# Kernel optimization log

Measured on AMD Instinct MI355X. Metric: run time of the kernel, lower is better.

Reference implementation:

```python
import jax, jax.numpy as jnp
import numpy as np

# MUCMA: multiuser CMA adaptive MIMO FIR equalizer (commplax af.mucma)
# framed_signal: (N, taps, dims) complex, carried as re/im float32 pairs.
N, TAPS, DIMS, DELTA = 131072, 19, 2, 6
LR = 2.0 ** (-13)
BETA = 0.999
R2 = 1.32  # E|a|^4 / E|a|^2 for unit-power 16QAM constellation


def setup_inputs() -> dict:
    key = jax.random.key(0)
    k1, k2 = jax.random.split(key)
    fr_re = jax.random.normal(k1, (N, TAPS, DIMS), dtype=jnp.float32) * 0.7071
    fr_im = jax.random.normal(k2, (N, TAPS, DIMS), dtype=jnp.float32) * 0.7071
    # initial MIMO weights: identity at the center tap (commplax mucma init)
    w0_re = np.zeros((DIMS, DIMS, TAPS), dtype=np.float32)
    ctap = (TAPS + 1) // 2 - 1
    w0_re[np.arange(DIMS), np.arange(DIMS), ctap] = 1.0
    return {
        'fr_re': fr_re,
        'fr_im': fr_im,
        'w0_re': jnp.asarray(w0_re),
        'w0_im': jnp.zeros((DIMS, DIMS, TAPS), jnp.float32),
    }


def _mucma_forward(fr_re, fr_im, w0_re, w0_im):
    u_all = fr_re + 1j * fr_im                      # (N, taps, dims) complex64
    w0 = (w0_re + 1j * w0_im).astype(u_all.dtype)   # (dims, dims, taps)
    # mask kills self cross-correlation terms (k == l)
    mask = (1.0 - jnp.eye(DIMS, dtype=jnp.float32))[:, :, None]

    def step(carry, u):
        # u: (taps, dims) frame of input samples
        w, z, r, bp = carry
        v = jnp.einsum('ijt,tj->i', w, u)                     # MIMO FIR output, (dims,)
        z = jnp.concatenate((v[None, :], z[:-1]))             # output delay line, (delta, dims)
        # running cross-correlation r[k,l,d] ~ E[z_k(n) z_l(n-d)^*]
        r = BETA * r + (1.0 - BETA) * jnp.einsum('k,dl->kld', v, z.conj())
        rhat = (r / (1.0 - bp)) * mask                        # bias-corrected, off-diagonal only
        e = R2 - jnp.abs(v) ** 2                              # CMA modulus error, (dims,) real
        loss = jnp.sum(e ** 2) + 2.0 * jnp.sum(jnp.abs(rhat) ** 2)
        uc = u.conj().T[None, :, :]                           # (1, dims, taps)
        g_cma = -2.0 * e[:, None, None] * v[:, None, None] * uc
        g_mu = 2.0 * jnp.einsum('kld,dl->k', rhat, z.conj())[:, None, None] * uc
        w_new = w - LR * (g_cma + g_mu)
        bp = bp * BETA
        # emit the weights USED for this symbol (pre-update), as commplax does
        return (w_new, z, r, bp), (w, loss)

    z0 = jnp.zeros((DELTA, DIMS), u_all.dtype)
    r0 = jnp.zeros((DIMS, DIMS, DELTA), u_all.dtype)
    carry0 = (w0, z0, r0, jnp.float32(BETA))
    _, (ws, _losses) = jax.lax.scan(step, carry0, u_all)
    # apply: per-symbol MIMO filtering with the recorded weight trace
    sig = jnp.einsum('nijt,ntj->ni', ws, u_all)               # (N, dims) complex
    return jnp.stack([sig.real, sig.imag], axis=-1)           # (N, dims, 2) float32


def reference(fr_re, fr_im, w0_re, w0_im):
    return _mucma_forward(fr_re, fr_im, w0_re, w0_im)
```

## Files before the change

### kernel.cpp

```cpp
#include <hip/hip_runtime.h>


typedef float v2f __attribute__((ext_vector_type(2)));
typedef float v4f __attribute__((ext_vector_type(4), aligned(4)));

constexpr int   NTAPS  = 19;
constexpr int   FRST   = 38;
constexpr float BETA_C = 0.999f;
constexpr float OMB_C  = 0.001f;
constexpr float LR_C   = 0.0001220703125f;
constexpr float R2_C   = 1.32f;

template <int CTRL>
__device__ __forceinline__ float dpp_add(float x) {
    return x + __int_as_float(__builtin_amdgcn_update_dpp(
        0, __float_as_int(x), CTRL, 0xF, 0xF, true));
}
template <int CTRL>
__device__ __forceinline__ float dpp_mov(float x) {
    return __int_as_float(__builtin_amdgcn_update_dpp(
        0, __float_as_int(x), CTRL, 0xF, 0xF, true));
}
__device__ __forceinline__ float rowred_bcast(float x) {
    x = dpp_add<0x121>(x);
    x = dpp_add<0x122>(x);
    x = dpp_add<0x124>(x);
    x = dpp_add<0x128>(x);
    return x;
}
__device__ __forceinline__ void plane32_swap(float& a, float& b) {
    asm("s_nop 1\n\t"
        "v_permlane32_swap_b32 %0, %1\n\t"
        "s_nop 1"
        : "+v"(a), "+v"(b));
}

__global__ void __launch_bounds__(64, 1)
mucma_scan_kernel(const float* __restrict__ fr_re, const float* __restrict__ fr_im,
                  const float* __restrict__ w0r_in, const float* __restrict__ w0i_in,
                  float* __restrict__ out, int nsym)
{
    const int  lane = threadIdx.x;
    const int  sl   = lane & 31;
    const int  h    = lane >> 5;
    const int  loff = (4 * sl < 34) ? 4 * sl : 34;
    const float mA  = (sl <= 8) ? 1.f : 0.f;
    const float mB  = (sl <= 9) ? 1.f : 0.f;
    const bool d0f  = (sl == 10);
    const bool stf  = (sl == 0);

    v2f wA_r = {0.f,0.f}, wA_i = {0.f,0.f}, wB_r = {0.f,0.f}, wB_i = {0.f,0.f};
    if (sl <= 8) {
        const int b = h * FRST + 2 * sl;
        wA_r.x = w0r_in[b];         wA_r.y = w0r_in[b + NTAPS];
        wA_i.x = w0i_in[b];         wA_i.y = w0i_in[b + NTAPS];
        wB_r.x = w0r_in[b + 1];     wB_r.y = w0r_in[b + NTAPS + 1];
        wB_i.x = w0i_in[b + 1];     wB_i.y = w0i_in[b + NTAPS + 1];
    } else if (sl == 9) {
        wB_r.x = w0r_in[h * FRST + 18];  wB_r.y = w0r_in[h * FRST + 37];
        wB_i.x = w0i_in[h * FRST + 18];  wB_i.y = w0i_in[h * FRST + 37];
    }
    float r_re = 0.f, r_im = 0.f, z_re = 0.f, z_im = 0.f;
    float bp = BETA_C;

    bool csel;
    {
        const float own = h ? 11.f : 7.f;
        float v = own, X = own;
        plane32_swap(X, v);
        csel = (X != own);
    }

    const float* pre = fr_re + loff;
    const float* pim = fr_im + loff;

    v4f rr[8], ri[8];
#pragma unroll
    for (int p = 0; p < 8; ++p) {
        const int idx = (p < nsym) ? p : (nsym - 1);
        rr[p] = *(const v4f*)(pre + (size_t)idx * FRST);
        ri[p] = *(const v4f*)(pim + (size_t)idx * FRST);
    }

    auto body = [&](int n, int p, int npf) {
        const v4f uR = rr[p], uI = ri[p];
        rr[p] = *(const v4f*)(pre + (size_t)npf * FRST);
        ri[p] = *(const v4f*)(pim + (size_t)npf * FRST);

        const v2f uA_r = {uR.x, uR.y}, uB_r = {uR.z, uR.w};
        const v2f uA_i = {uI.x, uI.y}, uB_i = {uI.z, uI.w};

        v2f tr = wA_r * uA_r - wA_i * uA_i + wB_r * uB_r - wB_i * uB_i;
        v2f ti = wA_r * uA_i + wA_i * uA_r + wB_r * uB_i + wB_i * uB_r;
        float xr = tr.x + tr.y;
        float xi = ti.x + ti.y;
        xr = rowred_bcast(xr);
        xi = rowred_bcast(xi);
        const float vkr = xr, vki = xi;

        float Xr = xr, Xi = xi;
        plane32_swap(Xr, xr);
        plane32_swap(Xi, xi);
        const float vlr = csel ? Xr : xr;
        const float vli = csel ? Xi : xi;

        const float zsr = dpp_mov<0x111>(z_re);
        const float zsi = dpp_mov<0x111>(z_im);
        z_re = d0f ? vlr : zsr;
        z_im = d0f ? vli : zsi;

        const float ar = OMB_C * vkr, ai = OMB_C * vki;
        r_re = BETA_C * r_re + (ar * z_re + ai * z_im);
        r_im = BETA_C * r_im + (ai * z_re - ar * z_im);

        float qr = r_re * z_re + r_im * z_im;
        float qi = r_im * z_re - r_re * z_im;
        qr = rowred_bcast(qr);
        qi = rowred_bcast(qi);

        const float inv = __builtin_amdgcn_rcpf(1.0f - bp);
        bp *= BETA_C;
        const float i2 = (2.0f * LR_C) * inv;
        const float ek = R2_C - (vkr * vkr + vki * vki);
        const float e2 = (-2.0f * LR_C) * ek;
        const float cr = e2 * vkr + i2 * qr;
        const float ci = e2 * vki + i2 * qi;

        const float crA = cr * mA, ciA = ci * mA;
        const float crB = cr * mB, ciB = ci * mB;
        const v2f cAr = {crA, crA}, cAi = {ciA, ciA};
        const v2f cBr = {crB, crB}, cBi = {ciB, ciB};
        wA_r -= cAr * uA_r + cAi * uA_i;
        wA_i -= cAi * uA_r - cAr * uA_i;
        wB_r -= cBr * uB_r + cBi * uB_i;
        wB_i -= cBi * uB_r - cBr * uB_i;

        if (stf) {
            v2f o; o.x = vkr; o.y = vki;
            *(v2f*)(out + 4 * (size_t)n + 2 * h) = o;
        }
    };

    int NBmain = nsym / 8 - 1;
    if (NBmain < 0) NBmain = 0;
    for (int b = 0; b < NBmain; ++b) {
        const int nb = b * 8;
#pragma unroll
        for (int p = 0; p < 8; ++p) body(nb + p, p, nb + p + 8);
    }
    for (int nb = NBmain * 8; nb < nsym; nb += 8) {
#pragma unroll
        for (int p = 0; p < 8; ++p) {
            const int n = nb + p;
            if (n < nsym) {
                int npf = n + 8;
                if (npf > nsym - 1) npf = nsym - 1;
                body(n, p, npf);
            }
        }
    }
}

extern "C" void kernel_launch(void* const* d_in, const int* in_sizes, int n_in,
                              void* d_out, int out_size, void* d_ws, size_t ws_size,
                              hipStream_t stream)
{
    const float* fr_re = (const float*)d_in[0];
    const float* fr_im = (const float*)d_in[1];
    const float* w0r   = (const float*)d_in[2];
    const float* w0i   = (const float*)d_in[3];
    float* outp = (float*)d_out;
    const int nsym = in_sizes[0] / FRST;
    hipLaunchKernelGGL(mucma_scan_kernel, dim3(1), dim3(64), 0, stream,
                       fr_re, fr_im, w0r, w0i, outp, nsym);
}
```

Measured before the change: 29.79 ms.

## Precompute frame Gram correlations to pipeline FIR output across scan steps

Adds a parallel pre-pass that computes the inner product between consecutive input frames, S[n] = <u_n, u_{n+1}>. The scan then computes the next symbol's FIR output from the pre-update weights and corrects it algebraically with the rank-one update term (c * S), which takes the reduction for v off the serial dependency chain. After SPLIT_N steps it also drops the bias-correction reciprocal, treating 1/(1-beta^n) as 1. That shortcut is an approximation whose error depends on the step count, and the new pre-pass is an extra kernel launch that needs workspace memory.

New measurement: 29.66 ms. Within noise of the previous version (-0.4%).

```diff
diff --git a/kernel.cpp b/kernel.cpp
--- a/kernel.cpp
+++ b/kernel.cpp
@@ -2,14 +2,15 @@
 
 
 typedef float v2f __attribute__((ext_vector_type(2)));
-typedef float v4f __attribute__((ext_vector_type(4), aligned(4)));
-
-constexpr int   NTAPS  = 19;
-constexpr int   FRST   = 38;
-constexpr float BETA_C = 0.999f;
-constexpr float OMB_C  = 0.001f;
-constexpr float LR_C   = 0.0001220703125f;
-constexpr float R2_C   = 1.32f;
+typedef float v4f __attribute__((ext_vector_type(4), aligned(8)));
+
+constexpr int   NTAPS   = 19;
+constexpr int   FRST    = 38;
+constexpr float BETA_C  = 0.999f;
+constexpr float OMB_C   = 0.001f;
+constexpr float LR_C    = 0.0001220703125f;
+constexpr float R2_C    = 1.32f;
+constexpr int   SPLIT_N = 24576;
 
 template <int CTRL>
 __device__ __forceinline__ float dpp_add(float x) {
@@ -34,130 +35,220 @@
         "s_nop 1"
         : "+v"(a), "+v"(b));
 }
+__device__ __forceinline__ void plane32_swap2(float& a, float& b, float& c, float& d) {
+    asm("s_nop 1\n\t"
+        "v_permlane32_swap_b32 %0, %1\n\t"
+        "v_permlane32_swap_b32 %2, %3\n\t"
+        "s_nop 1"
+        : "+v"(a), "+v"(b), "+v"(c), "+v"(d));
+}
+
+__global__ void __launch_bounds__(64)
+gram_kernel(const float* __restrict__ fr_re, const float* __restrict__ fr_im,
+            v2f* __restrict__ S, int nsym)
+{
+    __shared__ float lre[65 * FRST], lim[65 * FRST];
+    const int lane = threadIdx.x;
+    const int n0   = blockIdx.x * 64;
+    const int gmax = nsym * FRST;
+    for (int idx = lane; idx < 65 * FRST; idx += 64) {
+        const int g = n0 * FRST + idx;
+        if (g < gmax) { lre[idx] = fr_re[g]; lim[idx] = fr_im[g]; }
+    }
+    __syncthreads();
+    const int n = n0 + lane;
+    if (n >= nsym) return;
+    v2f s = {0.f, 0.f};
+    if (n + 1 < nsym) {
+        const float* ar = lre + lane * FRST;
+        const float* ai = lim + lane * FRST;
+        const float* br = ar + FRST;
+        const float* bi = ai + FRST;
+#pragma unroll
+        for (int e = 0; e < FRST; ++e) {
+            s.x += ar[e] * br[e] + ai[e] * bi[e];
+            s.y += ar[e] * bi[e] - ai[e] * br[e];
+        }
+    }
+    S[n] = s;
+}
+
+struct LaneCtx {
+    const float* pre; const float* pim; const v2f* Sb; float* out;
+    float mA, mB; bool d0f, stf, csel; int h;
+};
+struct ScanSt {
+    v2f  wA_r, wA_i, wB_r, wB_i;
+    float r_re, r_im, z_re, z_im, bp;
+    float Ar, Ai;
+    float cpr, cpi;
+    v2f  sp;
+    v4f  rr[8], ri[8];
+    v2f  sr[8];
+};
+
+template <bool EARLY, int P>
+__device__ __forceinline__ void mstep(int n, int npf, const LaneCtx& L, ScanSt& s)
+{
+    constexpr int PN = (P + 1) & 7;
+    const v4f uR  = s.rr[P],  uI  = s.ri[P];
+    const v4f u1R = s.rr[PN], u1I = s.ri[PN];
+    s.rr[P] = *(const v4f*)(L.pre + (size_t)npf * FRST);
+    s.ri[P] = *(const v4f*)(L.pim + (size_t)npf * FRST);
+    const v2f Scur = s.sr[P];
+    s.sr[P] = L.Sb[npf];
+
+    const v2f uA_r = {u1R.x, u1R.y}, uB_r = {u1R.z, u1R.w};
+    const v2f uA_i = {u1I.x, u1I.y}, uB_i = {u1I.z, u1I.w};
+    v2f tr = s.wA_r * uA_r - s.wA_i * uA_i + s.wB_r * uB_r - s.wB_i * uB_i;
+    v2f ti = s.wA_r * uA_i + s.wA_i * uA_r + s.wB_r * uB_i + s.wB_i * uB_r;
+    float nAr = tr.x + tr.y;
+    float nAi = ti.x + ti.y;
+    nAr = rowred_bcast(nAr);
+    nAi = rowred_bcast(nAi);
+
+    const float vkr = s.Ar - (s.cpr * s.sp.x - s.cpi * s.sp.y);
+    const float vki = s.Ai - (s.cpr * s.sp.y + s.cpi * s.sp.x);
+
+    if (L.stf) {
+        v2f o; o.x = vkr; o.y = vki;
+        *(v2f*)(L.out + 4 * (size_t)n + 2 * L.h) = o;
+    }
+
+    float Xr = vkr, Yr = vkr, Xi = vki, Yi = vki;
+    plane32_swap2(Xr, Yr, Xi, Yi);
+    const float vlr = L.csel ? Xr : Yr;
+    const float vli = L.csel ? Xi : Yi;
+
+    const float zsr = dpp_mov<0x111>(s.z_re);
+    const float zsi = dpp_mov<0x111>(s.z_im);
+    s.z_re = L.d0f ? vlr : zsr;
+    s.z_im = L.d0f ? vli : zsi;
+
+    const float ar = OMB_C * vkr, ai = OMB_C * vki;
+    s.r_re = BETA_C * s.r_re + (ar * s.z_re + ai * s.z_im);
+    s.r_im = BETA_C * s.r_im + (ai * s.z_re - ar * s.z_im);
+
+    float qr = s.r_re * s.z_re + s.r_im * s.z_im;
+    float qi = s.r_im * s.z_re - s.r_re * s.z_im;
+    qr = rowred_bcast(qr);
+    qi = rowred_bcast(qi);
+
+    float i2;
+    if (EARLY) {
+        const float inv = __builtin_amdgcn_rcpf(1.0f - s.bp);
+        s.bp *= BETA_C;
+        i2 = (2.0f * LR_C) * inv;
+    } else {
+        i2 = 2.0f * LR_C;
+    }
+    const float t  = vkr * vkr + vki * vki;
+    const float e2 = fmaf(2.0f * LR_C, t, -(2.0f * LR_C) * R2_C);
+    const float cr = fmaf(e2, vkr, i2 * qr);
+    const float ci = fmaf(e2, vki, i2 * qi);
+
+    const float crA = cr * L.mA, ciA = ci * L.mA;
+    const float crB = cr * L.mB, ciB = ci * L.mB;
+    const v2f uA_r0 = {uR.x, uR.y}, uB_r0 = {uR.z, uR.w};
+    const v2f uA_i0 = {uI.x, uI.y}, uB_i0 = {uI.z, uI.w};
+    const v2f cAr = {crA, crA}, cAi = {ciA, ciA};
+    const v2f cBr = {crB, crB}, cBi = {ciB, ciB};
+    s.wA_r -= cAr * uA_r0 + cAi * uA_i0;
+    s.wA_i -= cAi * uA_r0 - cAr * uA_i0;
+    s.wB_r -= cBr * uB_r0 + cBi * uB_i0;
+    s.wB_i -= cBi * uB_r0 - cBr * uB_i0;
+
+    s.Ar = nAr; s.Ai = nAi; s.cpr = cr; s.cpi = ci; s.sp = Scur;
+}
+
+template <bool EARLY>
+__device__ __forceinline__ void block8(int nb, const LaneCtx& L, ScanSt& s) {
+    mstep<EARLY, 0>(nb + 0, nb + 8,  L, s);
+    mstep<EARLY, 1>(nb + 1, nb + 9,  L, s);
+    mstep<EARLY, 2>(nb + 2, nb + 10, L, s);
+    mstep<EARLY, 3>(nb + 3, nb + 11, L, s);
+    mstep<EARLY, 4>(nb + 4, nb + 12, L, s);
+    mstep<EARLY, 5>(nb + 5, nb + 13, L, s);
+    mstep<EARLY, 6>(nb + 6, nb + 14, L, s);
+    mstep<EARLY, 7>(nb + 7, nb + 15, L, s);
+}
+template <bool EARLY>
+__device__ __forceinline__ void block8c(int nb, int nsym, const LaneCtx& L, ScanSt& s) {
+    const int last = nsym - 1;
+#define STEPC(K) { const int n = nb + K; if (n < nsym) { \
+        int npf = n + 8; if (npf > last) npf = last; mstep<EARLY, K>(n, npf, L, s); } }
+    STEPC(0) STEPC(1) STEPC(2) STEPC(3) STEPC(4) STEPC(5) STEPC(6) STEPC(7)
+#undef STEPC
+}
 
 __global__ void __launch_bounds__(64, 1)
 mucma_scan_kernel(const float* __restrict__ fr_re, const float* __restrict__ fr_im,
                   const float* __restrict__ w0r_in, const float* __restrict__ w0i_in,
-                  float* __restrict__ out, int nsym)
-{
-    const int  lane = threadIdx.x;
-    const int  sl   = lane & 31;
-    const int  h    = lane >> 5;
-    const int  loff = (4 * sl < 34) ? 4 * sl : 34;
-    const float mA  = (sl <= 8) ? 1.f : 0.f;
-    const float mB  = (sl <= 9) ? 1.f : 0.f;
-    const bool d0f  = (sl == 10);
-    const bool stf  = (sl == 0);
-
-    v2f wA_r = {0.f,0.f}, wA_i = {0.f,0.f}, wB_r = {0.f,0.f}, wB_i = {0.f,0.f};
-    if (sl <= 8) {
-        const int b = h * FRST + 2 * sl;
-        wA_r.x = w0r_in[b];         wA_r.y = w0r_in[b + NTAPS];
-        wA_i.x = w0i_in[b];         wA_i.y = w0i_in[b + NTAPS];
-        wB_r.x = w0r_in[b + 1];     wB_r.y = w0r_in[b + NTAPS + 1];
-        wB_i.x = w0i_in[b + 1];     wB_i.y = w0i_in[b + NTAPS + 1];
-    } else if (sl == 9) {
-        wB_r.x = w0r_in[h * FRST + 18];  wB_r.y = w0r_in[h * FRST + 37];
-        wB_i.x = w0i_in[h * FRST + 18];  wB_i.y = w0i_in[h * FRST + 37];
-    }
-    float r_re = 0.f, r_im = 0.f, z_re = 0.f, z_im = 0.f;
-    float bp = BETA_C;
-
-    bool csel;
+                  const v2f* __restrict__ Sbuf, float* __restrict__ out, int nsym)
+{
+    const int lane = threadIdx.x;
+    const int sl   = lane & 31;
+    const int h    = lane >> 5;
+    const int loff = (4 * sl < 34) ? 4 * sl : 34;
+
+    LaneCtx L;
+    L.pre = fr_re + loff;  L.pim = fr_im + loff;  L.Sb = Sbuf;  L.out = out;
+    L.mA  = (sl <= 8) ? 1.f : 0.f;
+    L.mB  = (sl <= 9) ? 1.f : 0.f;
+    L.d0f = (sl == 10);
+    L.stf = (sl == 0);
+    L.h   = h;
     {
         const float own = h ? 11.f : 7.f;
         float v = own, X = own;
         plane32_swap(X, v);
-        csel = (X != own);
-    }
-
-    const float* pre = fr_re + loff;
-    const float* pim = fr_im + loff;
-
-    v4f rr[8], ri[8];
+        L.csel = (X != own);
+    }
+
+    ScanSt s;
+    s.wA_r = {0.f,0.f}; s.wA_i = {0.f,0.f}; s.wB_r = {0.f,0.f}; s.wB_i = {0.f,0.f};
+    if (sl <= 8) {
+        const int b = h * FRST + 2 * sl;
+        s.wA_r.x = w0r_in[b];       s.wA_r.y = w0r_in[b + NTAPS];
+        s.wA_i.x = w0i_in[b];       s.wA_i.y = w0i_in[b + NTAPS];
+        s.wB_r.x = w0r_in[b + 1];   s.wB_r.y = w0r_in[b + NTAPS + 1];
+        s.wB_i.x = w0i_in[b + 1];   s.wB_i.y = w0i_in[b + NTAPS + 1];
+    } else if (sl == 9) {
+        s.wB_r.x = w0r_in[h * FRST + 18];  s.wB_r.y = w0r_in[h * FRST + 37];
+        s.wB_i.x = w0i_in[h * FRST + 18];  s.wB_i.y = w0i_in[h * FRST + 37];
+    }
+    s.r_re = 0.f; s.r_im = 0.f; s.z_re = 0.f; s.z_im = 0.f;
+    s.bp = BETA_C;
+    s.cpr = 0.f; s.cpi = 0.f; s.sp = {0.f, 0.f};
+
 #pragma unroll
     for (int p = 0; p < 8; ++p) {
         const int idx = (p < nsym) ? p : (nsym - 1);
-        rr[p] = *(const v4f*)(pre + (size_t)idx * FRST);
-        ri[p] = *(const v4f*)(pim + (size_t)idx * FRST);
-    }
-
-    auto body = [&](int n, int p, int npf) {
-        const v4f uR = rr[p], uI = ri[p];
-        rr[p] = *(const v4f*)(pre + (size_t)npf * FRST);
-        ri[p] = *(const v4f*)(pim + (size_t)npf * FRST);
-
+        s.rr[p] = *(const v4f*)(L.pre + (size_t)idx * FRST);
+        s.ri[p] = *(const v4f*)(L.pim + (size_t)idx * FRST);
+        s.sr[p] = Sbuf[idx];
+    }
+    {
+        const v4f uR = s.rr[0], uI = s.ri[0];
         const v2f uA_r = {uR.x, uR.y}, uB_r = {uR.z, uR.w};
         const v2f uA_i = {uI.x, uI.y}, uB_i = {uI.z, uI.w};
-
-        v2f tr = wA_r * uA_r - wA_i * uA_i + wB_r * uB_r - wB_i * uB_i;
-        v2f ti = wA_r * uA_i + wA_i * uA_r + wB_r * uB_i + wB_i * uB_r;
-        float xr = tr.x + tr.y;
-        float xi = ti.x + ti.y;
-        xr = rowred_bcast(xr);
-        xi = rowred_bcast(xi);
-        const float vkr = xr, vki = xi;
-
-        float Xr = xr, Xi = xi;
-        plane32_swap(Xr, xr);
-        plane32_swap(Xi, xi);
-        const float vlr = csel ? Xr : xr;
-        const float vli = csel ? Xi : xi;
-
-        const float zsr = dpp_mov<0x111>(z_re);
-        const float zsi = dpp_mov<0x111>(z_im);
-        z_re = d0f ? vlr : zsr;
-        z_im = d0f ? vli : zsi;
-
-        const float ar = OMB_C * vkr, ai = OMB_C * vki;
-        r_re = BETA_C * r_re + (ar * z_re + ai * z_im);
-        r_im = BETA_C * r_im + (ai * z_re - ar * z_im);
-
-        float qr = r_re * z_re + r_im * z_im;
-        float qi = r_im * z_re - r_re * z_im;
-        qr = rowred_bcast(qr);
-        qi = rowred_bcast(qi);
-
-        const float inv = __builtin_amdgcn_rcpf(1.0f - bp);
-        bp *= BETA_C;
-        const float i2 = (2.0f * LR_C) * inv;
-        const float ek = R2_C - (vkr * vkr + vki * vki);
-        const float e2 = (-2.0f * LR_C) * ek;
-        const float cr = e2 * vkr + i2 * qr;
-        const float ci = e2 * vki + i2 * qi;
-
-        const float crA = cr * mA, ciA = ci * mA;
-        const float crB = cr * mB, ciB = ci * mB;
-        const v2f cAr = {crA, crA}, cAi = {ciA, ciA};
-        const v2f cBr = {crB, crB}, cBi = {ciB, ciB};
-        wA_r -= cAr * uA_r + cAi * uA_i;
-        wA_i -= cAi * uA_r - cAr * uA_i;
-        wB_r -= cBr * uB_r + cBi * uB_i;
-        wB_i -= cBi * uB_r - cBr * uB_i;
-
-        if (stf) {
-            v2f o; o.x = vkr; o.y = vki;
-            *(v2f*)(out + 4 * (size_t)n + 2 * h) = o;
-        }
-    };
-
-    int NBmain = nsym / 8 - 1;
-    if (NBmain < 0) NBmain = 0;
-    for (int b = 0; b < NBmain; ++b) {
-        const int nb = b * 8;
-#pragma unroll
-        for (int p = 0; p < 8; ++p) body(nb + p, p, nb + p + 8);
-    }
-    for (int nb = NBmain * 8; nb < nsym; nb += 8) {
-#pragma unroll
-        for (int p = 0; p < 8; ++p) {
-            const int n = nb + p;
-            if (n < nsym) {
-                int npf = n + 8;
-                if (npf > nsym - 1) npf = nsym - 1;
-                body(n, p, npf);
-            }
-        }
+        v2f tr = s.wA_r * uA_r - s.wA_i * uA_i + s.wB_r * uB_r - s.wB_i * uB_i;
+        v2f ti = s.wA_r * uA_i + s.wA_i * uA_r + s.wB_r * uB_i + s.wB_i * uB_r;
+        s.Ar = rowred_bcast(tr.x + tr.y);
+        s.Ai = rowred_bcast(ti.x + ti.y);
+    }
+
+    if (nsym >= SPLIT_N + 16) {
+        for (int nb = 0; nb < SPLIT_N; nb += 8)
+            block8<true>(nb, L, s);
+        const int nmain = (nsym - 8) & ~7;
+        for (int nb = SPLIT_N; nb < nmain; nb += 8)
+            block8<false>(nb, L, s);
+        for (int nb = nmain; nb < nsym; nb += 8)
+            block8c<false>(nb, nsym, L, s);
+    } else {
+        for (int nb = 0; nb < nsym; nb += 8)
+            block8c<true>(nb, nsym, L, s);
     }
 }
 
@@ -170,7 +261,11 @@
     const float* w0r   = (const float*)d_in[2];
     const float* w0i   = (const float*)d_in[3];
     float* outp = (float*)d_out;
+    v2f*   Sbuf = (v2f*)d_ws;
     const int nsym = in_sizes[0] / FRST;
+
+    hipLaunchKernelGGL(gram_kernel, dim3((nsym + 63) / 64), dim3(64), 0, stream,
+                       fr_re, fr_im, Sbuf, nsym);
     hipLaunchKernelGGL(mucma_scan_kernel, dim3(1), dim3(64), 0, stream,
-                       fr_re, fr_im, w0r, w0i, outp, nsym);
-}
+                       fr_re, fr_im, w0r, w0i, Sbuf, outp, nsym);
+}
```

## Split sequential scan into two pipelined waves using precomputed frame Gram terms

Applied to the files above, without the earlier changes.

Adds a parallel pre-pass that computes lagged inner products between consecutive input frames (lags 1-3). The serial scan then runs as two wavefronts. One wave applies the filter with weights that lag by a few symbols and corrects the output using those inner products and the recent update coefficients. The other wave does the error, cross-correlation and coefficient work, and the two hand values to each other through LDS rings with a barrier per symbol. This is meant to take the weight update and filter reduction off the critical serial dependency chain. After SPLIT_N symbols it also drops the bias-correction reciprocal, treating 1-bp as 1, which is only approximately exact. It needs workspace, and the per-step barrier adds synchronisation cost.

New measurement: 29.44 ms. About the same (-1.2%).

```diff
diff --git a/kernel.cpp b/kernel.cpp
--- a/kernel.cpp
+++ b/kernel.cpp
@@ -1,15 +1,17 @@
 #include <hip/hip_runtime.h>
+#include <stdint.h>
 
 
 typedef float v2f __attribute__((ext_vector_type(2)));
-typedef float v4f __attribute__((ext_vector_type(4), aligned(4)));
-
-constexpr int   NTAPS  = 19;
-constexpr int   FRST   = 38;
-constexpr float BETA_C = 0.999f;
-constexpr float OMB_C  = 0.001f;
-constexpr float LR_C   = 0.0001220703125f;
-constexpr float R2_C   = 1.32f;
+typedef float v4f __attribute__((ext_vector_type(4), aligned(8)));
+
+constexpr int   NTAPS   = 19;
+constexpr int   FRST    = 38;
+constexpr float BETA_C  = 0.999f;
+constexpr float OMB_C   = 0.001f;
+constexpr float LR_C    = 0.0001220703125f;
+constexpr float R2_C    = 1.32f;
+constexpr int   SPLIT_N = 24576;
 
 template <int CTRL>
 __device__ __forceinline__ float dpp_add(float x) {
@@ -34,11 +36,316 @@
         "s_nop 1"
         : "+v"(a), "+v"(b));
 }
+__device__ __forceinline__ void plane32_swap2(float& a, float& b, float& c, float& d) {
+    asm("s_nop 1\n\t"
+        "v_permlane32_swap_b32 %0, %1\n\t"
+        "v_permlane32_swap_b32 %2, %3\n\t"
+        "s_nop 1"
+        : "+v"(a), "+v"(b), "+v"(c), "+v"(d));
+}
+__device__ __forceinline__ void wg_barrier() {
+    asm volatile("s_waitcnt lgkmcnt(0)\n\ts_barrier" ::: "memory");
+}
+
+__global__ void __launch_bounds__(64)
+gram3_kernel(const float* __restrict__ fr_re, const float* __restrict__ fr_im,
+             char* __restrict__ ws, int nsym)
+{
+    v4f* SA4 = (v4f*)ws;
+    v2f* SA2 = (v2f*)(ws + (size_t)nsym * 16);
+    __shared__ float lre[67 * FRST], lim[67 * FRST];
+    const int lane = threadIdx.x;
+    const int n0   = blockIdx.x * 64;
+    const long gmax = (long)nsym * FRST;
+    for (int idx = lane; idx < 67 * FRST; idx += 64) {
+        const long g = (long)n0 * FRST + idx;
+        if (g < gmax) { lre[idx] = fr_re[g]; lim[idx] = fr_im[g]; }
+    }
+    __syncthreads();
+    const int n = n0 + lane;
+    if (n >= nsym) return;
+    const float* ar = lre + lane * FRST;
+    const float* ai = lim + lane * FRST;
+    v2f s1 = {0.f,0.f}, s2 = {0.f,0.f}, s3 = {0.f,0.f};
+#pragma unroll
+    for (int e = 0; e < FRST; ++e) {
+        const float xr = ar[e], xi = ai[e];
+        const float b1r = ar[e+FRST],   b1i = ai[e+FRST];
+        const float b2r = ar[e+2*FRST], b2i = ai[e+2*FRST];
+        const float b3r = ar[e+3*FRST], b3i = ai[e+3*FRST];
+        s1.x += xr*b1r + xi*b1i;  s1.y += xr*b1i - xi*b1r;
+        s2.x += xr*b2r + xi*b2i;  s2.y += xr*b2i - xi*b2r;
+        s3.x += xr*b3r + xi*b3i;  s3.y += xr*b3i - xi*b3r;
+    }
+    if (n + 1 >= nsym) s1 = (v2f){0.f,0.f};
+    if (n + 2 >= nsym) s2 = (v2f){0.f,0.f};
+    if (n + 3 >= nsym) s3 = (v2f){0.f,0.f};
+    SA4[n] = (v4f){s1.x, s1.y, s2.x, s2.y};
+    SA2[n] = s3;
+}
+
+struct AS {
+    float araw_r, araw_i;
+    float cp1r, cp1i, cp2r, cp2i, cp3r, cp3i;
+    float z_re, z_im, r_re, r_im, bp;
+    v4f sa4[8]; v2f sa2[8];
+    const v4f* pa40; const v2f* pa20;
+    const v4f* pa4;  const v2f* pa2;
+    float* stb; int stadv;
+};
+
+template <bool EARLY, int P>
+__device__ __forceinline__ void A_step(AS& s, const v4f* p4, const v2f* p2,
+                                       float* sp, float* cw, const float* ard,
+                                       bool d0f, bool csel)
+{
+    const v4f S1e = s.sa4[(P+7)&7];
+    const v4f S2e = s.sa4[(P+6)&7];
+    const v2f S3e = s.sa2[(P+5)&7];
+
+    float vr = s.araw_r - (s.cp1r*S1e.x - s.cp1i*S1e.y)
+                        - (s.cp2r*S2e.z - s.cp2i*S2e.w)
+                        - (s.cp3r*S3e.x - s.cp3i*S3e.y);
+    float vi = s.araw_i - (s.cp1r*S1e.y + s.cp1i*S1e.x)
+                        - (s.cp2r*S2e.w + s.cp2i*S2e.z)
+                        - (s.cp3r*S3e.y + s.cp3i*S3e.x);
+
+    const v2f an = *(const v2f*)(ard + ((P+1)&7)*4);
+
+    *(v2f*)sp = (v2f){vr, vi};
+
+    float Xr = vr, Yr = vr, Xi = vi, Yi = vi;
+    plane32_swap2(Xr, Yr, Xi, Yi);
+    const float vlr = csel ? Xr : Yr;
+    const float vli = csel ? Xi : Yi;
+
+    const float zsr = dpp_mov<0x111>(s.z_re);
+    const float zsi = dpp_mov<0x111>(s.z_im);
+    s.z_re = d0f ? vlr : zsr;
+    s.z_im = d0f ? vli : zsi;
+
+    const float ar = OMB_C * vr, ai = OMB_C * vi;
+    s.r_re = BETA_C * s.r_re + (ar * s.z_re + ai * s.z_im);
+    s.r_im = BETA_C * s.r_im + (ai * s.z_re - ar * s.z_im);
+
+    float qr = s.r_re * s.z_re + s.r_im * s.z_im;
+    float qi = s.r_im * s.z_re - s.r_re * s.z_im;
+    qr = rowred_bcast(qr);
+    qi = rowred_bcast(qi);
+
+    float i2;
+    if (EARLY) {
+        const float inv = __builtin_amdgcn_rcpf(1.0f - s.bp);
+        s.bp *= BETA_C;
+        i2 = (2.0f * LR_C) * inv;
+    } else {
+        i2 = 2.0f * LR_C;
+    }
+    const float t  = vr*vr + vi*vi;
+    const float e2 = fmaf(2.0f*LR_C, t, -(2.0f*LR_C)*R2_C);
+    const float cr = fmaf(e2, vr, i2*qr);
+    const float ci = fmaf(e2, vi, i2*qi);
+
+    *(v2f*)(cw + P*4) = (v2f){cr, ci};
+
+    s.cp3r = s.cp2r; s.cp3i = s.cp2i;
+    s.cp2r = s.cp1r; s.cp2i = s.cp1i;
+    s.cp1r = cr;     s.cp1i = ci;
+    s.araw_r = an.x; s.araw_i = an.y;
+
+    s.sa4[(P+5)&7] = p4[0];
+    s.sa2[(P+5)&7] = p2[0];
+}
+
+template <bool EARLY, bool TAIL>
+__device__ __forceinline__ void a_block(AS& s, int nb, int last,
+    float* cw, const float* ard, bool d0f, bool csel, float* gdl)
+{
+#define ASTP(P) { \
+    const v4f* p4; const v2f* p2; float* sp; \
+    if (TAIL) { int rfi = nb + P + 5; if (rfi > last) rfi = last; \
+                p4 = s.pa40 + rfi; p2 = s.pa20 + rfi; \
+                sp = (nb + P <= last) ? (s.stb + P*4) : (gdl + P*4); } \
+    else { p4 = s.pa4 + (P+5); p2 = s.pa2 + (P+5); sp = s.stb + P*4; } \
+    A_step<EARLY, P>(s, p4, p2, sp, cw, ard, d0f, csel); \
+    wg_barrier(); }
+    ASTP(0) ASTP(1) ASTP(2) ASTP(3) ASTP(4) ASTP(5) ASTP(6) ASTP(7)
+#undef ASTP
+    s.pa4 += 8; s.pa2 += 8; s.stb += s.stadv;
+}
+
+struct BS {
+    v2f wA_r, wA_i, wB_r, wB_i;
+    v4f rr[8], ri[8];
+    v4f uo_r, uo_i;
+    float cregr, cregi;
+    const float* ubr; const float* ubi;
+    float mA, mB;
+};
+
+__device__ __forceinline__ v2f b_tree(const BS& s, const v4f& uR, const v4f& uI) {
+    const v2f uA_r = {uR.x,uR.y}, uB_r = {uR.z,uR.w};
+    const v2f uA_i = {uI.x,uI.y}, uB_i = {uI.z,uI.w};
+    v2f tr = s.wA_r*uA_r - s.wA_i*uA_i + s.wB_r*uB_r - s.wB_i*uB_i;
+    v2f ti = s.wA_r*uA_i + s.wA_i*uA_r + s.wB_r*uB_i + s.wB_i*uB_r;
+    return (v2f){ rowred_bcast(tr.x + tr.y), rowred_bcast(ti.x + ti.y) };
+}
+
+template <int P>
+__device__ __forceinline__ void B_step(BS& s, const float* urf_re, const float* urf_im,
+                                       const float* crd, float* aw)
+{
+    const v2f cn = *(const v2f*)(crd + ((P+7)&7)*4);
+
+    const float crA = s.cregr * s.mA, ciA = s.cregi * s.mA;
+    const float crB = s.cregr * s.mB, ciB = s.cregi * s.mB;
+    {
+        const v2f uA_r = {s.uo_r.x, s.uo_r.y}, uB_r = {s.uo_r.z, s.uo_r.w};
+        const v2f uA_i = {s.uo_i.x, s.uo_i.y}, uB_i = {s.uo_i.z, s.uo_i.w};
+        s.wA_r -= (v2f){crA,crA}*uA_r + (v2f){ciA,ciA}*uA_i;
+        s.wA_i -= (v2f){ciA,ciA}*uA_r - (v2f){crA,crA}*uA_i;
+        s.wB_r -= (v2f){crB,crB}*uB_r + (v2f){ciB,ciB}*uB_i;
+        s.wB_i -= (v2f){ciB,ciB}*uB_r - (v2f){crB,crB}*uB_i;
+    }
+    {
+        const v2f T = b_tree(s, s.rr[(P+2)&7], s.ri[(P+2)&7]);
+        *(v2f*)(aw + ((P+2)&7)*4) = T;
+    }
+    s.uo_r = s.rr[(P+7)&7];
+    s.uo_i = s.ri[(P+7)&7];
+    s.rr[(P+7)&7] = *(const v4f*)urf_re;
+    s.ri[(P+7)&7] = *(const v4f*)urf_im;
+    s.cregr = cn.x; s.cregi = cn.y;
+}
+
+template <bool TAIL>
+__device__ __forceinline__ void b_block(BS& s, int nb, int last,
+    const float* fr_re, const float* fr_im, int loff,
+    const float* crd, float* aw)
+{
+#define BSTP(P) { \
+    const float* ur; const float* ui2; \
+    if (TAIL) { int rfi = nb + P + 7; if (rfi > last) rfi = last; \
+                ur  = fr_re + (size_t)rfi * FRST + loff; \
+                ui2 = fr_im + (size_t)rfi * FRST + loff; } \
+    else { ur = s.ubr + P*FRST; ui2 = s.ubi + P*FRST; } \
+    B_step<P>(s, ur, ui2, crd, aw); \
+    wg_barrier(); }
+    BSTP(0) BSTP(1) BSTP(2) BSTP(3) BSTP(4) BSTP(5) BSTP(6) BSTP(7)
+#undef BSTP
+    s.ubr += 8*FRST; s.ubi += 8*FRST;
+}
+
+__global__ void __launch_bounds__(128, 1)
+mucma2_kernel(const float* __restrict__ fr_re, const float* __restrict__ fr_im,
+              const float* __restrict__ w0r_in, const float* __restrict__ w0i_in,
+              char* __restrict__ ws, float* __restrict__ out, int nsym)
+{
+    __shared__ __align__(16) float cring[8][2][2];
+    __shared__ __align__(16) float aring[8][2][2];
+    __shared__ __align__(16) float ldsd[2048];
+
+    const int  tid  = threadIdx.x;
+    const int  wid  = tid >> 6;
+    const int  lane = tid & 63;
+    const int  sl   = lane & 31;
+    const int  h    = lane >> 5;
+    const int  loff = (4*sl < 34) ? 4*sl : 34;
+    const bool d0f  = (sl == 10);
+    const bool stf  = (sl == 0);
+    const int  last = nsym - 1;
+
+    bool csel;
+    { const float own = h ? 11.f : 7.f; float v = own, X = own;
+      plane32_swap(X, v); csel = (X != own); }
+
+    int NBm = (nsym - 14) / 8; if (NBm < 0) NBm = 0;
+    const int nmain = NBm * 8;
+    const int ne    = (SPLIT_N < nmain) ? SPLIT_N : nmain;
+
+    if (wid == 0) {
+        if (lane < 32) ((float*)cring)[lane] = 0.f;
+        else           ((float*)aring)[lane - 32] = 0.f;
+        wg_barrier();
+        wg_barrier();
+
+        AS s;
+        uintptr_t a4u = (uintptr_t)ws;                     asm volatile("" : "+v"(a4u));
+        uintptr_t a2u = (uintptr_t)(ws + (size_t)nsym*16); asm volatile("" : "+v"(a2u));
+        s.pa40 = (const v4f*)a4u; s.pa20 = (const v2f*)a2u;
+        s.pa4 = s.pa40; s.pa2 = s.pa20;
+#pragma unroll
+        for (int k = 0; k < 8; ++k) {
+            const int idx = (k < 5) ? ((k <= last) ? k : last) : 0;
+            s.sa4[k] = s.pa40[idx];
+            s.sa2[k] = s.pa20[idx];
+        }
+        float* gdum = (float*)(ws + (size_t)nsym*24);
+        float* gdl  = gdum + lane*32;
+        s.stb   = stf ? (out + 2*h) : gdl;
+        s.stadv = stf ? 32 : 0;
+        s.cp1r=0.f; s.cp1i=0.f; s.cp2r=0.f; s.cp2i=0.f; s.cp3r=0.f; s.cp3i=0.f;
+        s.z_re=0.f; s.z_im=0.f; s.r_re=0.f; s.r_im=0.f; s.bp = BETA_C;
+        { const v2f a0 = *(const v2f*)&aring[0][h][0]; s.araw_r = a0.x; s.araw_i = a0.y; }
+        float* cw = stf ? &cring[0][h][0] : &ldsd[lane*32];
+        const float* ard = &aring[0][h][0];
+
+        for (int nb = 0;  nb < ne;    nb += 8) a_block<true , false>(s, nb, last, cw, ard, d0f, csel, gdl);
+        for (int nb = ne; nb < nmain; nb += 8) a_block<false, false>(s, nb, last, cw, ard, d0f, csel, gdl);
+        if (nmain < SPLIT_N)
+            for (int nb = nmain; nb < nsym; nb += 8) a_block<true , true>(s, nb, last, cw, ard, d0f, csel, gdl);
+        else
+            for (int nb = nmain; nb < nsym; nb += 8) a_block<false, true>(s, nb, last, cw, ard, d0f, csel, gdl);
+    } else {
+        BS s;
+        s.mA = (sl <= 8) ? 1.f : 0.f;
+        s.mB = (sl <= 9) ? 1.f : 0.f;
+        s.wA_r = (v2f){0.f,0.f}; s.wA_i = (v2f){0.f,0.f};
+        s.wB_r = (v2f){0.f,0.f}; s.wB_i = (v2f){0.f,0.f};
+        if (sl <= 8) {
+            const int b = h*FRST + 2*sl;
+            s.wA_r.x = w0r_in[b];       s.wA_r.y = w0r_in[b+NTAPS];
+            s.wA_i.x = w0i_in[b];       s.wA_i.y = w0i_in[b+NTAPS];
+            s.wB_r.x = w0r_in[b+1];     s.wB_r.y = w0r_in[b+NTAPS+1];
+            s.wB_i.x = w0i_in[b+1];     s.wB_i.y = w0i_in[b+NTAPS+1];
+        } else if (sl == 9) {
+            s.wB_r.x = w0r_in[h*FRST+18];  s.wB_r.y = w0r_in[h*FRST+37];
+            s.wB_i.x = w0i_in[h*FRST+18];  s.wB_i.y = w0i_in[h*FRST+37];
+        }
+        const float* pre = fr_re + loff;
+        const float* pim = fr_im + loff;
+#pragma unroll
+        for (int k = 0; k < 7; ++k) {
+            const int idx = (k <= last) ? k : last;
+            s.rr[k] = *(const v4f*)(pre + (size_t)idx*FRST);
+            s.ri[k] = *(const v4f*)(pim + (size_t)idx*FRST);
+        }
+        s.rr[7] = (v4f){0.f,0.f,0.f,0.f}; s.ri[7] = (v4f){0.f,0.f,0.f,0.f};
+        s.uo_r  = (v4f){0.f,0.f,0.f,0.f}; s.uo_i  = (v4f){0.f,0.f,0.f,0.f};
+        s.cregr = 0.f; s.cregi = 0.f;
+        s.ubr = pre + (size_t)7*FRST;
+        s.ubi = pim + (size_t)7*FRST;
+        float* aw = stf ? &aring[0][h][0] : &ldsd[lane*32 + 2];
+        const float* crd = &cring[0][h][0];
+
+        wg_barrier();
+        {
+            const v2f T0 = b_tree(s, s.rr[0], s.ri[0]);
+            *(v2f*)(aw + 0) = T0;
+            const v2f T1 = b_tree(s, s.rr[1], s.ri[1]);
+            *(v2f*)(aw + 4) = T1;
+        }
+        wg_barrier();
+
+        for (int nb = 0;     nb < nmain; nb += 8) b_block<false>(s, nb, last, fr_re, fr_im, loff, crd, aw);
+        for (int nb = nmain; nb < nsym;  nb += 8) b_block<true >(s, nb, last, fr_re, fr_im, loff, crd, aw);
+    }
+}
 
 __global__ void __launch_bounds__(64, 1)
-mucma_scan_kernel(const float* __restrict__ fr_re, const float* __restrict__ fr_im,
-                  const float* __restrict__ w0r_in, const float* __restrict__ w0i_in,
-                  float* __restrict__ out, int nsym)
+mucma_scan_fb(const float* __restrict__ fr_re, const float* __restrict__ fr_im,
+              const float* __restrict__ w0r_in, const float* __restrict__ w0i_in,
+              float* __restrict__ out, int nsym)
 {
     const int  lane = threadIdx.x;
     const int  sl   = lane & 31;
@@ -47,7 +354,7 @@
     const float mA  = (sl <= 8) ? 1.f : 0.f;
     const float mB  = (sl <= 9) ? 1.f : 0.f;
     const bool d0f  = (sl == 10);
-    const bool stf  = (sl == 0);
+    const bool stfl = (sl == 0);
 
     v2f wA_r = {0.f,0.f}, wA_i = {0.f,0.f}, wB_r = {0.f,0.f}, wB_i = {0.f,0.f};
     if (sl <= 8) {
@@ -92,10 +399,8 @@
 
         v2f tr = wA_r * uA_r - wA_i * uA_i + wB_r * uB_r - wB_i * uB_i;
         v2f ti = wA_r * uA_i + wA_i * uA_r + wB_r * uB_i + wB_i * uB_r;
-        float xr = tr.x + tr.y;
-        float xi = ti.x + ti.y;
-        xr = rowred_bcast(xr);
-        xi = rowred_bcast(xi);
+        float xr = rowred_bcast(tr.x + tr.y);
+        float xi = rowred_bcast(ti.x + ti.y);
         const float vkr = xr, vki = xi;
 
         float Xr = xr, Xi = xi;
@@ -128,14 +433,12 @@
 
         const float crA = cr * mA, ciA = ci * mA;
         const float crB = cr * mB, ciB = ci * mB;
-        const v2f cAr = {crA, crA}, cAi = {ciA, ciA};
-        const v2f cBr = {crB, crB}, cBi = {ciB, ciB};
-        wA_r -= cAr * uA_r + cAi * uA_i;
-        wA_i -= cAi * uA_r - cAr * uA_i;
-        wB_r -= cBr * uB_r + cBi * uB_i;
-        wB_i -= cBi * uB_r - cBr * uB_i;
-
-        if (stf) {
+        wA_r -= (v2f){crA,crA} * uA_r + (v2f){ciA,ciA} * uA_i;
+        wA_i -= (v2f){ciA,ciA} * uA_r - (v2f){crA,crA} * uA_i;
+        wB_r -= (v2f){crB,crB} * uB_r + (v2f){ciB,ciB} * uB_i;
+        wB_i -= (v2f){ciB,ciB} * uB_r - (v2f){crB,crB} * uB_i;
+
+        if (stfl) {
             v2f o; o.x = vkr; o.y = vki;
             *(v2f*)(out + 4 * (size_t)n + 2 * h) = o;
         }
@@ -171,6 +474,15 @@
     const float* w0i   = (const float*)d_in[3];
     float* outp = (float*)d_out;
     const int nsym = in_sizes[0] / FRST;
-    hipLaunchKernelGGL(mucma_scan_kernel, dim3(1), dim3(64), 0, stream,
-                       fr_re, fr_im, w0r, w0i, outp, nsym);
-}
+
+    const size_t need = (size_t)nsym * 24 + 64 * 1024;
+    if (ws_size >= need && nsym >= 16) {
+        hipLaunchKernelGGL(gram3_kernel, dim3((nsym + 63) / 64), dim3(64), 0, stream,
+                           fr_re, fr_im, (char*)d_ws, nsym);
+        hipLaunchKernelGGL(mucma2_kernel, dim3(1), dim3(128), 0, stream,
+                           fr_re, fr_im, w0r, w0i, (char*)d_ws, outp, nsym);
+    } else {
+        hipLaunchKernelGGL(mucma_scan_fb, dim3(1), dim3(64), 0, stream,
+                           fr_re, fr_im, w0r, w0i, outp, nsym);
+    }
+}
```

## Split scan into lagged-weight pipeline with precomputed frame Gram terms

Applied to the files above, without the earlier changes.

Adds a parallel pre-pass that computes inner products between each frame and its 7 predecessors. The serial scan then becomes a two-wave producer/consumer pipeline. One wave computes outputs from stale-weight FIR results corrected through the Gram terms and past update coefficients. The other wave applies the weight updates and computes FIR outputs several symbols ahead, with the two exchanging data through LDS rings and barriers. Past a fixed symbol index the bias-correction factor is treated as one, which removes the reciprocal from the critical path but approximates 1/(1-beta^n). This is meant to shorten the per-symbol dependency chain, at the cost of an extra kernel, workspace traffic and per-four-symbol barriers.

New measurement: 27.11 ms. 9.0% less time.

```diff
diff --git a/kernel.cpp b/kernel.cpp
--- a/kernel.cpp
+++ b/kernel.cpp
@@ -1,15 +1,17 @@
 #include <hip/hip_runtime.h>
+#include <stdint.h>
 
 
 typedef float v2f __attribute__((ext_vector_type(2)));
-typedef float v4f __attribute__((ext_vector_type(4), aligned(4)));
-
-constexpr int   NTAPS  = 19;
-constexpr int   FRST   = 38;
-constexpr float BETA_C = 0.999f;
-constexpr float OMB_C  = 0.001f;
-constexpr float LR_C   = 0.0001220703125f;
-constexpr float R2_C   = 1.32f;
+typedef float v4f __attribute__((ext_vector_type(4), aligned(8)));
+
+constexpr int   NTAPS   = 19;
+constexpr int   FRST    = 38;
+constexpr float BETA_C  = 0.999f;
+constexpr float OMB_C   = 0.001f;
+constexpr float LR_C    = 0.0001220703125f;
+constexpr float R2_C    = 1.32f;
+constexpr int   SPLIT_N = 24576;
 
 template <int CTRL>
 __device__ __forceinline__ float dpp_add(float x) {
@@ -34,11 +36,309 @@
         "s_nop 1"
         : "+v"(a), "+v"(b));
 }
+__device__ __forceinline__ void plane32_swap2(float& a, float& b, float& c, float& d) {
+    asm("s_nop 1\n\t"
+        "v_permlane32_swap_b32 %0, %1\n\t"
+        "v_permlane32_swap_b32 %2, %3\n\t"
+        "s_nop 1"
+        : "+v"(a), "+v"(b), "+v"(c), "+v"(d));
+}
+__device__ __forceinline__ void wg_barrier() {
+    asm volatile("s_waitcnt lgkmcnt(0)\n\ts_barrier" ::: "memory");
+}
+
+__global__ void __launch_bounds__(64)
+gram7_kernel(const float* __restrict__ fr_re, const float* __restrict__ fr_im,
+             float* __restrict__ sc, int nsym)
+{
+    __shared__ float lre[71 * FRST], lim[71 * FRST];
+    const int lane = threadIdx.x;
+    const int n0   = blockIdx.x * 64;
+    const int base = (n0 - 7) * FRST;
+    const long gmax = (long)nsym * FRST;
+    for (int idx = lane; idx < 71 * FRST; idx += 64) {
+        const long g = (long)base + idx;
+        float a = 0.f, b = 0.f;
+        if (g >= 0 && g < gmax) { a = fr_re[g]; b = fr_im[g]; }
+        lre[idx] = a; lim[idx] = b;
+    }
+    __syncthreads();
+    const int m = n0 + lane;
+    if (m >= nsym) return;
+    const float* br = lre + (lane + 7) * FRST;
+    const float* bi = lim + (lane + 7) * FRST;
+    float out[16];
+#pragma unroll
+    for (int k = 1; k <= 7; ++k) {
+        const float* ar = br - k * FRST;
+        const float* ai = bi - k * FRST;
+        float sr = 0.f, si = 0.f;
+#pragma unroll
+        for (int e = 0; e < FRST; ++e) {
+            sr = fmaf(ar[e], br[e], fmaf(ai[e], bi[e], sr));
+            si = fmaf(-ai[e], br[e], fmaf(ar[e], bi[e], si));
+        }
+        const bool ok = (m >= k);
+        out[2*(k-1)]   = ok ? sr : 0.f;
+        out[2*(k-1)+1] = ok ? si : 0.f;
+    }
+    out[14] = 0.f; out[15] = 0.f;
+    float* d = sc + (size_t)m * 16;
+#pragma unroll
+    for (int j = 0; j < 4; ++j)
+        *(v4f*)(d + 4*j) = (v4f){out[4*j], out[4*j+1], out[4*j+2], out[4*j+3]};
+}
+
+struct A_St {
+    float acr[8], aci[8];
+    float histr[8], histi[8];
+    v4f   scr[4][4];
+    float z_re, z_im, r_re, r_im, bp;
+};
+struct A_Ctx {
+    const float* scp; float* outp;
+    float (*aring)[2][32][2]; float (*cring)[2][32][2];
+    int h, sl; bool d0f, csel; int last;
+};
+
+template <int S, bool EARLY, bool TAIL>
+__device__ __forceinline__ void a_pos(A_St& st, const A_Ctx& c, int SB)
+{
+    constexpr int s8 = S & 7, s4 = S & 3, NC = 4 + (S & 3);
+    const int m = SB + S;
+
+    float vr = st.acr[s8], vi = st.aci[s8];
+#pragma unroll
+    for (int k = 1; k <= NC; ++k) {
+        const float hr = st.histr[(S - k) & 7];
+        const float hi = st.histi[(S - k) & 7];
+        const v4f sv = st.scr[s4][(k - 1) >> 1];
+        const float Sr = (k & 1) ? sv.x : sv.z;
+        const float Si = (k & 1) ? sv.y : sv.w;
+        vr = fmaf(-hr, Sr, fmaf( hi, Si, vr));
+        vi = fmaf(-hr, Si, fmaf(-hi, Sr, vi));
+    }
+
+    *(v2f*)(c.outp + 4 * (size_t)m + 2 * c.h) = (v2f){vr, vi};
+
+    float Xr = vr, Yr = vr, Xi = vi, Yi = vi;
+    plane32_swap2(Xr, Yr, Xi, Yi);
+    const float vlr = c.csel ? Xr : Yr;
+    const float vli = c.csel ? Xi : Yi;
+
+    const float zsr = dpp_mov<0x111>(st.z_re);
+    const float zsi = dpp_mov<0x111>(st.z_im);
+    st.z_re = c.d0f ? vlr : zsr;
+    st.z_im = c.d0f ? vli : zsi;
+
+    const float ar = OMB_C * vr, ai = OMB_C * vi;
+    st.r_re = BETA_C * st.r_re + (ar * st.z_re + ai * st.z_im);
+    st.r_im = BETA_C * st.r_im + (ai * st.z_re - ar * st.z_im);
+
+    float qr = st.r_re * st.z_re + st.r_im * st.z_im;
+    float qi = st.r_im * st.z_re - st.r_re * st.z_im;
+    qr = rowred_bcast(qr);
+    qi = rowred_bcast(qi);
+
+    float i2;
+    if (EARLY) {
+        const float inv = __builtin_amdgcn_rcpf(1.0f - st.bp);
+        st.bp *= BETA_C;
+        i2 = (2.0f * LR_C) * inv;
+    } else {
+        i2 = 2.0f * LR_C;
+    }
+    const float t  = vr * vr + vi * vi;
+    const float e2 = fmaf(2.0f * LR_C, t, -(2.0f * LR_C) * R2_C);
+    const float cr = fmaf(e2, vr, i2 * qr);
+    const float ci = fmaf(e2, vi, i2 * qi);
+
+    st.histr[s8] = cr; st.histi[s8] = ci;
+    *(v2f*)&c.cring[s8][c.h][c.sl][0] = (v2f){cr, ci};
+
+    int mp = m + 4;
+    if (TAIL) { if (mp > c.last) mp = c.last; }
+    const float* p = c.scp + (size_t)mp * 16;
+#pragma unroll
+    for (int j = 0; j < 4; ++j)
+        st.scr[s4][j] = *(const v4f*)(p + 4 * j);
+}
+
+template <int I, bool EARLY, bool TAIL>
+__device__ __forceinline__ void a_sub(A_St& st, const A_Ctx& c, int SB)
+{
+#pragma unroll
+    for (int t = 0; t < 4; ++t) {
+        const v2f a0 = *(const v2f*)&c.aring[(4*I + t) & 7][c.h][0][0];
+        st.acr[(4*I + t) & 7] = a0.x;
+        st.aci[(4*I + t) & 7] = a0.y;
+    }
+    a_pos<4*I + 0, EARLY, TAIL>(st, c, SB);
+    a_pos<4*I + 1, EARLY, TAIL>(st, c, SB);
+    a_pos<4*I + 2, EARLY, TAIL>(st, c, SB);
+    a_pos<4*I + 3, EARLY, TAIL>(st, c, SB);
+    wg_barrier();
+}
+template <bool EARLY, bool TAIL>
+__device__ __forceinline__ void a_super(A_St& st, const A_Ctx& c, int SB)
+{
+    a_sub<0, EARLY, TAIL>(st, c, SB);
+    a_sub<1, EARLY, TAIL>(st, c, SB);
+    a_sub<2, EARLY, TAIL>(st, c, SB);
+    a_sub<3, EARLY, TAIL>(st, c, SB);
+}
+
+struct B_St {
+    v2f wA_r, wA_i, wB_r, wB_i;
+    v4f ur[16], ui[16];
+    float mA, mB;
+};
+struct B_Ctx {
+    const float* pre; const float* pim;
+    float (*aring)[2][32][2]; float (*cring)[2][32][2];
+    int h, sl; int last;
+};
+
+__device__ __forceinline__ v2f b_tree(const B_St& s, const v4f& uR, const v4f& uI) {
+    const v2f uA_r = {uR.x,uR.y}, uB_r = {uR.z,uR.w};
+    const v2f uA_i = {uI.x,uI.y}, uB_i = {uI.z,uI.w};
+    v2f tr = s.wA_r*uA_r - s.wA_i*uA_i + s.wB_r*uB_r - s.wB_i*uB_i;
+    v2f ti = s.wA_r*uA_i + s.wA_i*uA_r + s.wB_r*uB_i + s.wB_i*uB_r;
+    return (v2f){ rowred_bcast(tr.x + tr.y), rowred_bcast(ti.x + ti.y) };
+}
+
+template <int I, bool TAIL>
+__device__ __forceinline__ void b_sub(B_St& st, const B_Ctx& c, int SB)
+{
+    float ccr[4], cci[4];
+#pragma unroll
+    for (int t = 0; t < 4; ++t) {
+        const v2f cc = *(const v2f*)&c.cring[(4*I + 4 + t) & 7][c.h][0][0];
+        ccr[t] = cc.x; cci[t] = cc.y;
+    }
+#pragma unroll
+    for (int t = 0; t < 4; ++t) {
+        const float crA = ccr[t] * st.mA, ciA = cci[t] * st.mA;
+        const float crB = ccr[t] * st.mB, ciB = cci[t] * st.mB;
+        const v4f uR = st.ur[(4*I + 12 + t) & 15], uI = st.ui[(4*I + 12 + t) & 15];
+        const v2f uA_r = {uR.x,uR.y}, uB_r = {uR.z,uR.w};
+        const v2f uA_i = {uI.x,uI.y}, uB_i = {uI.z,uI.w};
+        st.wA_r -= (v2f){crA,crA}*uA_r + (v2f){ciA,ciA}*uA_i;
+        st.wA_i -= (v2f){ciA,ciA}*uA_r - (v2f){crA,crA}*uA_i;
+        st.wB_r -= (v2f){crB,crB}*uB_r + (v2f){ciB,ciB}*uB_i;
+        st.wB_i -= (v2f){ciB,ciB}*uB_r - (v2f){crB,crB}*uB_i;
+    }
+#pragma unroll
+    for (int t = 0; t < 4; ++t) {
+        const v2f T = b_tree(st, st.ur[(4*I + 4 + t) & 15], st.ui[(4*I + 4 + t) & 15]);
+        *(v2f*)&c.aring[(4*I + 4 + t) & 7][c.h][c.sl][0] = T;
+    }
+#pragma unroll
+    for (int t = 0; t < 4; ++t) {
+        int f = SB + 4*I + 8 + t;
+        if (TAIL) { if (f > c.last) f = c.last; }
+        st.ur[(4*I + 8 + t) & 15] = *(const v4f*)(c.pre + (size_t)f * FRST);
+        st.ui[(4*I + 8 + t) & 15] = *(const v4f*)(c.pim + (size_t)f * FRST);
+    }
+    wg_barrier();
+}
+template <bool TAIL>
+__device__ __forceinline__ void b_super(B_St& st, const B_Ctx& c, int SB)
+{
+    b_sub<0, TAIL>(st, c, SB);
+    b_sub<1, TAIL>(st, c, SB);
+    b_sub<2, TAIL>(st, c, SB);
+    b_sub<3, TAIL>(st, c, SB);
+}
+
+__global__ void __launch_bounds__(128, 1)
+mucma2b_kernel(const float* __restrict__ fr_re, const float* __restrict__ fr_im,
+               const float* __restrict__ w0r_in, const float* __restrict__ w0i_in,
+               const float* __restrict__ scp, float* __restrict__ outp, int nsym)
+{
+    __shared__ __align__(16) float cring[8][2][32][2];
+    __shared__ __align__(16) float aring[8][2][32][2];
+
+    const int  tid  = threadIdx.x;
+    const int  wid  = tid >> 6;
+    const int  lane = tid & 63;
+    const int  sl   = lane & 31;
+    const int  h    = lane >> 5;
+    const int  loff = (4*sl < 34) ? 4*sl : 34;
+    const int  last = nsym - 1;
+    const int  SBend = nsym - 16;
+
+    bool csel;
+    { const float own = h ? 11.f : 7.f; float v = own, X = own;
+      plane32_swap(X, v); csel = (X != own); }
+
+    if (wid == 0) {
+        A_St st; A_Ctx c;
+        c.scp = scp; c.outp = outp; c.aring = aring; c.cring = cring;
+        c.h = h; c.sl = sl; c.d0f = ((sl & 15) == 10); c.csel = csel; c.last = last;
+#pragma unroll
+        for (int k = 0; k < 8; ++k) {
+            st.histr[k] = 0.f; st.histi[k] = 0.f;
+            st.acr[k] = 0.f;  st.aci[k] = 0.f;
+        }
+        st.z_re = 0.f; st.z_im = 0.f; st.r_re = 0.f; st.r_im = 0.f; st.bp = BETA_C;
+#pragma unroll
+        for (int s = 0; s < 4; ++s)
+#pragma unroll
+            for (int j = 0; j < 4; ++j)
+                st.scr[s][j] = *(const v4f*)(scp + (size_t)s * 16 + 4 * j);
+        if (lane < 32) cring[lane >> 2][(lane >> 1) & 1][0][lane & 1] = 0.f;
+        wg_barrier();
+
+        int SB = 0;
+        for (; SB < SPLIT_N; SB += 16) a_super<true , false>(st, c, SB);
+        for (; SB < SBend;   SB += 16) a_super<false, false>(st, c, SB);
+        a_super<false, true>(st, c, SB);
+    } else {
+        B_St st; B_Ctx c;
+        c.pre = fr_re + loff; c.pim = fr_im + loff;
+        c.aring = aring; c.cring = cring; c.h = h; c.sl = sl; c.last = last;
+        st.mA = (sl <= 8) ? 1.f : 0.f;
+        st.mB = (sl <= 9) ? 1.f : 0.f;
+        st.wA_r = (v2f){0.f,0.f}; st.wA_i = (v2f){0.f,0.f};
+        st.wB_r = (v2f){0.f,0.f}; st.wB_i = (v2f){0.f,0.f};
+        if (sl <= 8) {
+            const int b = h*FRST + 2*sl;
+            st.wA_r.x = w0r_in[b];       st.wA_r.y = w0r_in[b+NTAPS];
+            st.wA_i.x = w0i_in[b];       st.wA_i.y = w0i_in[b+NTAPS];
+            st.wB_r.x = w0r_in[b+1];     st.wB_r.y = w0r_in[b+NTAPS+1];
+            st.wB_i.x = w0i_in[b+1];     st.wB_i.y = w0i_in[b+NTAPS+1];
+        } else if (sl == 9) {
+            st.wB_r.x = w0r_in[h*FRST+18];  st.wB_r.y = w0r_in[h*FRST+37];
+            st.wB_i.x = w0i_in[h*FRST+18];  st.wB_i.y = w0i_in[h*FRST+37];
+        }
+#pragma unroll
+        for (int k = 0; k < 12; ++k) {
+            st.ur[k] = *(const v4f*)(c.pre + (size_t)k * FRST);
+            st.ui[k] = *(const v4f*)(c.pim + (size_t)k * FRST);
+        }
+#pragma unroll
+        for (int k = 12; k < 16; ++k) {
+            st.ur[k] = (v4f){0.f,0.f,0.f,0.f};
+            st.ui[k] = (v4f){0.f,0.f,0.f,0.f};
+        }
+#pragma unroll
+        for (int t = 0; t < 4; ++t) {
+            const v2f T = b_tree(st, st.ur[t], st.ui[t]);
+            *(v2f*)&aring[t][h][sl][0] = T;
+        }
+        wg_barrier();
+
+        int SB = 0;
+        for (; SB < SBend; SB += 16) b_super<false>(st, c, SB);
+        b_super<true>(st, c, SB);
+    }
+}
 
 __global__ void __launch_bounds__(64, 1)
-mucma_scan_kernel(const float* __restrict__ fr_re, const float* __restrict__ fr_im,
-                  const float* __restrict__ w0r_in, const float* __restrict__ w0i_in,
-                  float* __restrict__ out, int nsym)
+mucma_scan_fb(const float* __restrict__ fr_re, const float* __restrict__ fr_im,
+              const float* __restrict__ w0r_in, const float* __restrict__ w0i_in,
+              float* __restrict__ out, int nsym)
 {
     const int  lane = threadIdx.x;
     const int  sl   = lane & 31;
@@ -47,7 +347,7 @@
     const float mA  = (sl <= 8) ? 1.f : 0.f;
     const float mB  = (sl <= 9) ? 1.f : 0.f;
     const bool d0f  = (sl == 10);
-    const bool stf  = (sl == 0);
+    const bool stfl = (sl == 0);
 
     v2f wA_r = {0.f,0.f}, wA_i = {0.f,0.f}, wB_r = {0.f,0.f}, wB_i = {0.f,0.f};
     if (sl <= 8) {
@@ -92,10 +392,8 @@
 
         v2f tr = wA_r * uA_r - wA_i * uA_i + wB_r * uB_r - wB_i * uB_i;
         v2f ti = wA_r * uA_i + wA_i * uA_r + wB_r * uB_i + wB_i * uB_r;
-        float xr = tr.x + tr.y;
-        float xi = ti.x + ti.y;
-        xr = rowred_bcast(xr);
-        xi = rowred_bcast(xi);
+        float xr = rowred_bcast(tr.x + tr.y);
+        float xi = rowred_bcast(ti.x + ti.y);
         const float vkr = xr, vki = xi;
 
         float Xr = xr, Xi = xi;
@@ -128,14 +426,12 @@
 
         const float crA = cr * mA, ciA = ci * mA;
         const float crB = cr * mB, ciB = ci * mB;
-        const v2f cAr = {crA, crA}, cAi = {ciA, ciA};
-        const v2f cBr = {crB, crB}, cBi = {ciB, ciB};
-        wA_r -= cAr * uA_r + cAi * uA_i;
-        wA_i -= cAi * uA_r - cAr * uA_i;
-        wB_r -= cBr * uB_r + cBi * uB_i;
-        wB_i -= cBi * uB_r - cBr * uB_i;
-
-        if (stf) {
+        wA_r -= (v2f){crA,crA} * uA_r + (v2f){ciA,ciA} * uA_i;
+        wA_i -= (v2f){ciA,ciA} * uA_r - (v2f){crA,crA} * uA_i;
+        wB_r -= (v2f){crB,crB} * uB_r + (v2f){ciB,ciB} * uB_i;
+        wB_i -= (v2f){ciB,ciB} * uB_r - (v2f){crB,crB} * uB_i;
+
+        if (stfl) {
             v2f o; o.x = vkr; o.y = vki;
             *(v2f*)(out + 4 * (size_t)n + 2 * h) = o;
         }
@@ -171,6 +467,16 @@
     const float* w0i   = (const float*)d_in[3];
     float* outp = (float*)d_out;
     const int nsym = in_sizes[0] / FRST;
-    hipLaunchKernelGGL(mucma_scan_kernel, dim3(1), dim3(64), 0, stream,
-                       fr_re, fr_im, w0r, w0i, outp, nsym);
-}
+
+    const bool use2 = (nsym % 16 == 0) && (nsym >= SPLIT_N + 16)
+                   && (ws_size >= (size_t)nsym * 64);
+    if (use2) {
+        hipLaunchKernelGGL(gram7_kernel, dim3((nsym + 63) / 64), dim3(64), 0, stream,
+                           fr_re, fr_im, (float*)d_ws, nsym);
+        hipLaunchKernelGGL(mucma2b_kernel, dim3(1), dim3(128), 0, stream,
+                           fr_re, fr_im, w0r, w0i, (const float*)d_ws, outp, nsym);
+    } else {
+        hipLaunchKernelGGL(mucma_scan_fb, dim3(1), dim3(64), 0, stream,
+                           fr_re, fr_im, w0r, w0i, outp, nsym);
+    }
+}
```
